# Kernel tuning notes

Hardware: AMD Instinct MI355X
Metric: run time of the kernel (lower is better)

## Reference

```python
import jax, jax.numpy as jnp
import numpy as np
import math

B, N, Q, K = 1, 64, 512, 512
C_Q = C_K = C_V = 256
C_HIDDEN = 32
NO_HEADS = 8
HID = C_HIDDEN * NO_HEADS  # 256


def setup_inputs() -> dict:
    key = jax.random.key(0)
    ks = jax.random.split(key, 12)
    inp = {
        "q_x": jax.random.normal(ks[0], (B, N, Q, C_Q), jnp.float32),
        "k_x": jax.random.normal(ks[1], (B, N, K, C_K), jnp.float32),
        "v_x": jax.random.normal(ks[2], (B, N, K, C_V), jnp.float32),
        "bias_mask": jax.random.normal(ks[3], (B, N, 1, 1, K), jnp.float32),
        "bias_pair": jax.random.normal(ks[4], (B, 1, NO_HEADS, Q, K), jnp.float32),
        # projection weights stored [in, out] (torch Linear is [out, in])
        "wq": jax.random.normal(ks[5], (C_Q, HID), jnp.float32) / math.sqrt(C_Q),
        "wk": jax.random.normal(ks[6], (C_K, HID), jnp.float32) / math.sqrt(C_K),
        "wv": jax.random.normal(ks[7], (C_V, HID), jnp.float32) / math.sqrt(C_V),
        # gating: init weights=0, bias=1 in the module; use small random for a non-trivial test
        "wg": jax.random.normal(ks[8], (C_Q, HID), jnp.float32) * 0.02,
        "bg": jnp.ones((HID,), jnp.float32),
        # output: init 'final' (zeros); use small random for a non-trivial test
        "wo": jax.random.normal(ks[9], (HID, C_Q), jnp.float32) * 0.02,
        "bo": jnp.zeros((C_Q,), jnp.float32),
    }
    return inp


def reference(q_x, k_x, v_x, bias_mask, bias_pair, wq, wk, wv, wg, bg, wo, bo):
    h, c = NO_HEADS, C_HIDDEN
    # projections -> [B, N, Q/K, H, C_h]
    q = (q_x @ wq).reshape(*q_x.shape[:-1], h, c) / math.sqrt(c)
    k = (k_x @ wk).reshape(*k_x.shape[:-1], h, c)
    v = (v_x @ wv).reshape(*v_x.shape[:-1], h, c)
    # logits [B, N, H, Q, K] with additive biases
    a = jnp.einsum("bnqhc,bnkhc->bnhqk", q, k) + bias_mask + bias_pair
    a = jax.nn.softmax(a, axis=-1)
    # output [B, N, Q, H, C_h]
    o = jnp.einsum("bnhqk,bnkhc->bnqhc", a, v)
    # gating
    g = jax.nn.sigmoid((q_x @ wg + bg).reshape(*q_x.shape[:-1], h, c))
    o = o * g
    o = o.reshape(*o.shape[:-2], h * c)
    return o @ wo + bo
```

## Files before the change

kernel.cpp:

```cpp
#include <hip/hip_runtime.h>
#include <math.h>

#define NSEQ   64
#define QLEN   512
#define KLEN   512
#define CIN    256
#define HEADS  8
#define CH     32
#define HIDDIM 256
#define M_TOTAL (NSEQ * QLEN)
#define L2E    1.4426950408889634f

typedef _Float16 f16x8 __attribute__((ext_vector_type(8)));
typedef _Float16 f16x4 __attribute__((ext_vector_type(4)));
typedef __fp16   fp16x2 __attribute__((ext_vector_type(2)));
typedef float    f32x4 __attribute__((ext_vector_type(4)));

__device__ __forceinline__ void gload16(const void* g, void* l) {
    __builtin_amdgcn_global_load_lds(
        (const __attribute__((address_space(1))) void*)g,
        (__attribute__((address_space(3))) void*)l, 16, 0, 0);
}

__device__ __forceinline__ float exp2_fast(float x) {
#if __has_builtin(__builtin_amdgcn_exp2f)
    return __builtin_amdgcn_exp2f(x);
#else
    float r; asm("v_exp_f32 %0, %1" : "=v"(r) : "v"(x)); return r;
#endif
}

__global__ __launch_bounds__(256) void wcast_kernel(
    const float* __restrict__ w0, const float* __restrict__ w1,
    const float* __restrict__ w2, const float* __restrict__ w3,
    const float* __restrict__ w4, const float* __restrict__ bm,
    float* __restrict__ bm2, _Float16* __restrict__ wt)
{
    if (blockIdx.z == 5) {
        const int id = ((blockIdx.y * 4 + blockIdx.x) * 256 + threadIdx.x) * 8;
        float4 a = *(const float4*)(bm + id);
        float4 b = *(const float4*)(bm + id + 4);
        a.x *= L2E; a.y *= L2E; a.z *= L2E; a.w *= L2E;
        b.x *= L2E; b.y *= L2E; b.z *= L2E; b.w *= L2E;
        *(float4*)(bm2 + id) = a;
        *(float4*)(bm2 + id + 4) = b;
        return;
    }
    __shared__ float t[64][65];
    const float* W;
    switch (blockIdx.z) {
        case 0: W = w0; break; case 1: W = w1; break;
        case 2: W = w2; break; case 3: W = w3; break;
        default: W = w4;
    }
    _Float16* WT = wt + (size_t)blockIdx.z * 65536;
    const int i0 = blockIdx.x * 64, o0 = blockIdx.y * 64;
    const int tid = threadIdx.x;
    const int rr = tid >> 4, c4 = tid & 15;
    #pragma unroll
    for (int i = 0; i < 4; ++i) {
        const int row = rr + i * 16;
        *(float4*)&t[row][c4 * 4] = *(const float4*)&W[(size_t)(i0 + row) * 256 + o0 + c4 * 4];
    }
    __syncthreads();
    #pragma unroll
    for (int i = 0; i < 4; ++i) {
        const int row = rr + i * 16;
        f16x4 v;
        #pragma unroll
        for (int j = 0; j < 4; ++j) v[j] = (_Float16)t[c4 * 4 + j][row];
        *(f16x4*)&WT[(size_t)(o0 + row) * 256 + i0 + c4 * 4] = v;
    }
}

__global__ __launch_bounds__(256) void bpfrag_kernel(
    const float* __restrict__ bias_pair, float* __restrict__ frag)
{
    __shared__ float t[64][68];
    const int qb = blockIdx.x, kb = blockIdx.y, h = blockIdx.z;
    const int tid = threadIdx.x;
    #pragma unroll
    for (int i = 0; i < 4; ++i) {
        const int idx = tid + i * 256;
        const int r = idx >> 4, c4 = idx & 15;
        *(float4*)&t[r][c4 * 4] = *(const float4*)
            &bias_pair[((size_t)h * QLEN + qb * 64 + r) * KLEN + kb * 64 + c4 * 4];
    }
    __syncthreads();
    const int lane = tid & 63, w = tid >> 6;
    const int l15 = lane & 15, quad = lane >> 4;
    const int qt = qb * 4 + w;
    #pragma unroll
    for (int kt2 = 0; kt2 < 4; ++kt2) {
        const int kt = kb * 4 + kt2;
        float4 v;
        v.x = (t[w * 16 + l15][kt2 * 16 + quad * 4 + 0] - 4.0f) * L2E;
        v.y = (t[w * 16 + l15][kt2 * 16 + quad * 4 + 1] - 4.0f) * L2E;
        v.z = (t[w * 16 + l15][kt2 * 16 + quad * 4 + 2] - 4.0f) * L2E;
        v.w = (t[w * 16 + l15][kt2 * 16 + quad * 4 + 3] - 4.0f) * L2E;
        *(float4*)&frag[(((size_t)(h * 32 + qt) * 32) + kt) * 256 + lane * 4] = v;
    }
}

__global__ __launch_bounds__(256, 3) void proj_gemm_kernel(
    const float* __restrict__ q_x, const float* __restrict__ k_x,
    const float* __restrict__ v_x, const _Float16* __restrict__ wT,
    const float* __restrict__ bg,
    _Float16* __restrict__ oq, _Float16* __restrict__ ok,
    _Float16* __restrict__ ovT, _Float16* __restrict__ og)
{
    __shared__ __attribute__((aligned(16))) _Float16 A_s[2][32 * 256];

    const int combo = blockIdx.x >> 7;
    const int blk   = blockIdx.x & 127;
    const int mode  = combo >> 1;
    const int nhalf = combo & 1;
    const float* A = (mode <= 1) ? q_x : (mode == 2) ? k_x : v_x;
    const _Float16* BT = wT + (size_t)mode * 65536;

    const int tid  = threadIdx.x;
    const int lane = tid & 63, w = tid >> 6;
    const int l15  = lane & 15, quad = lane >> 4;
    const int nw   = nhalf * 128 + w * 32;

    f16x8 bfr[2][8];
    #pragma unroll
    for (int nt = 0; nt < 2; ++nt)
        #pragma unroll
        for (int ks = 0; ks < 8; ++ks)
            bfr[nt][ks] = *(const f16x8*)(BT +
                (size_t)(nw + nt * 16 + l15) * 256 + ks * 32 + quad * 8);

    float4 bg4[2] = {{0.f,0.f,0.f,0.f},{0.f,0.f,0.f,0.f}};
    if (mode == 1) {
        bg4[0] = *(const float4*)&bg[nw + quad * 4];
        bg4[1] = *(const float4*)&bg[nw + 16 + quad * 4];
    }

    const int row_base = blk * 256;

    f32x4 acc[2][2];
    #pragma unroll
    for (int mt = 0; mt < 2; ++mt)
        #pragma unroll
        for (int nt = 0; nt < 2; ++nt) acc[mt][nt] = (f32x4){0.f, 0.f, 0.f, 0.f};

    float4 sreg[8];

    auto gload_panel = [&](int panel) {
        const int row0 = row_base + panel * 32;
        #pragma unroll
        for (int j = 0; j < 4; ++j) {
            const int p = tid + j * 256;
            const int r = p >> 5, c = p & 31;
            const float* ap = A + (size_t)(row0 + r) * 256 + c * 8;
            sreg[j * 2]     = *(const float4*)ap;
            sreg[j * 2 + 1] = *(const float4*)(ap + 4);
        }
    };

    auto swrite_panel = [&](int buf) {
        #pragma unroll
        for (int j = 0; j < 4; ++j) {
            const int p = tid + j * 256;
            const int r = p >> 5, c = p & 31;
            const int cp = c ^ (r & 15);
            f16x8 v;
            v[0] = (_Float16)sreg[j * 2].x;     v[1] = (_Float16)sreg[j * 2].y;
            v[2] = (_Float16)sreg[j * 2].z;     v[3] = (_Float16)sreg[j * 2].w;
            v[4] = (_Float16)sreg[j * 2 + 1].x; v[5] = (_Float16)sreg[j * 2 + 1].y;
            v[6] = (_Float16)sreg[j * 2 + 1].z; v[7] = (_Float16)sreg[j * 2 + 1].w;
            *(f16x8*)&A_s[buf][(r * 32 + cp) * 8] = v;
        }
    };

    gload_panel(0);
    swrite_panel(0);
    asm volatile("s_waitcnt lgkmcnt(0)" ::: "memory");
    __builtin_amdgcn_s_barrier();

    for (int i = 0; i < 8; ++i) {
        const int buf = i & 1;
        if (i < 7) gload_panel(i + 1);

        #pragma unroll
        for (int ks = 0; ks < 8; ++ks) {
            f16x8 af[2];
            #pragma unroll
            for (int mt = 0; mt < 2; ++mt) {
                const int r  = mt * 16 + l15;
                const int cp = (ks * 4 + quad) ^ (r & 15);
                af[mt] = *(const f16x8*)&A_s[buf][(r * 32 + cp) * 8];
            }
            if (mode != 3) {
                #pragma unroll
                for (int mt = 0; mt < 2; ++mt)
                    #pragma unroll
                    for (int nt = 0; nt < 2; ++nt)
                        acc[mt][nt] = __builtin_amdgcn_mfma_f32_16x16x32_f16(
                            bfr[nt][ks], af[mt], acc[mt][nt], 0, 0, 0);
            } else {
                #pragma unroll
                for (int mt = 0; mt < 2; ++mt)
                    #pragma unroll
                    for (int nt = 0; nt < 2; ++nt)
                        acc[mt][nt] = __builtin_amdgcn_mfma_f32_16x16x32_f16(
                            af[mt], bfr[nt][ks], acc[mt][nt], 0, 0, 0);
            }
        }

        const int row0 = row_base + i * 32;
        if (mode == 3) {
            #pragma unroll
            for (int mt = 0; mt < 2; ++mt) {
                #pragma unroll
                for (int nt = 0; nt < 2; ++nt) {
                    const int col  = nw + nt * 16 + l15;
                    const int rowg = row0 + mt * 16 + quad * 4;
                    const int nn = rowg >> 9, kpos = rowg & 511;
                    f16x4 st;
                    #pragma unroll
                    for (int reg = 0; reg < 4; ++reg) st[reg] = (_Float16)acc[mt][nt][reg];
                    *(f16x4*)&ovT[((size_t)(nn * 256 + col)) * 512 + kpos] = st;
                }
            }
        } else {
            _Float16* C = (mode == 0) ? oq : (mode == 1) ? og : ok;
            #pragma unroll
            for (int mt = 0; mt < 2; ++mt) {
                const int mrow = row0 + mt * 16 + l15;
                #pragma unroll
                for (int nt = 0; nt < 2; ++nt) {
                    const int colb = nw + nt * 16 + quad * 4;
                    f16x4 st;
                    #pragma unroll
                    for (int reg = 0; reg < 4; ++reg) {
                        float x = acc[mt][nt][reg];
                        if (mode == 0) x *= 0.2550348614f;
                        if (mode == 1) {
                            x += ((const float*)&bg4[nt])[reg];
                            x = 1.0f / (1.0f + __expf(-x));
                        }
                        st[reg] = (_Float16)x;
                    }
                    *(f16x4*)&C[(size_t)mrow * HIDDIM + colb] = st;
                }
            }
        }
        #pragma unroll
        for (int mt = 0; mt < 2; ++mt)
            #pragma unroll
            for (int nt = 0; nt < 2; ++nt) acc[mt][nt] = (f32x4){0.f, 0.f, 0.f, 0.f};

        if (i < 7) {
            swrite_panel(buf ^ 1);
            asm volatile("s_waitcnt lgkmcnt(0)" ::: "memory");
            __builtin_amdgcn_s_barrier();
        }
    }
}

__global__ __launch_bounds__(256, 4) void outproj_kernel(
    const _Float16* __restrict__ Ain, const _Float16* __restrict__ BT,
    const float* __restrict__ bias, float* __restrict__ Cout)
{
    __shared__ __attribute__((aligned(16))) _Float16 A_s[2][32 * 256];

    const int blk   = blockIdx.x & 511;
    const int nhalf = blockIdx.x >> 9;
    const int tid  = threadIdx.x;
    const int lane = tid & 63, w = tid >> 6;
    const int l15  = lane & 15, quad = lane >> 4;
    const int nw   = nhalf * 128 + w * 32;
    const int row_base = blk * 64;

    #pragma unroll
    for (int pan = 0; pan < 2; ++pan) {
        const int row0 = row_base + pan * 32;
        #pragma unroll
        for (int j = 0; j < 4; ++j) {
            const int p = tid + j * 256;
            const int r = p >> 5, c = p & 31;
            const int cl = (c & ~7) | ((c & 7) ^ (r & 7));
            gload16(Ain + (size_t)(row0 + r) * 256 + cl * 8, &A_s[pan][p * 8]);
        }
    }

    f16x8 bfr[2][8];
    #pragma unroll
    for (int nt = 0; nt < 2; ++nt)
        #pragma unroll
        for (int ks = 0; ks < 8; ++ks)
            bfr[nt][ks] = *(const f16x8*)(BT +
                (size_t)(nw + nt * 16 + l15) * 256 + ks * 32 + quad * 8);

    const float4 bias4[2] = {
        *(const float4*)&bias[nw + quad * 4],
        *(const float4*)&bias[nw + 16 + quad * 4],
    };

    __syncthreads();

    #pragma unroll
    for (int i = 0; i < 2; ++i) {
        f32x4 acc[2][2];
        #pragma unroll
        for (int mt = 0; mt < 2; ++mt)
            #pragma unroll
            for (int nt = 0; nt < 2; ++nt) acc[mt][nt] = (f32x4){0.f, 0.f, 0.f, 0.f};

        #pragma unroll
        for (int ks = 0; ks < 8; ++ks) {
            f16x8 af[2];
            #pragma unroll
            for (int mt = 0; mt < 2; ++mt) {
                const int r = mt * 16 + l15;
                const int c = (ks * 4 + quad) ^ (r & 7);
                af[mt] = *(const f16x8*)&A_s[i][r * 256 + c * 8];
            }
            #pragma unroll
            for (int mt = 0; mt < 2; ++mt)
                #pragma unroll
                for (int nt = 0; nt < 2; ++nt)
                    acc[mt][nt] = __builtin_amdgcn_mfma_f32_16x16x32_f16(
                        bfr[nt][ks], af[mt], acc[mt][nt], 0, 0, 0);
        }

        const int row0 = row_base + i * 32;
        #pragma unroll
        for (int mt = 0; mt < 2; ++mt) {
            const int mrow = row0 + mt * 16 + l15;
            #pragma unroll
            for (int nt = 0; nt < 2; ++nt) {
                const int colb = nw + nt * 16 + quad * 4;
                float4 st;
                st.x = acc[mt][nt][0] + bias4[nt].x;
                st.y = acc[mt][nt][1] + bias4[nt].y;
                st.z = acc[mt][nt][2] + bias4[nt].z;
                st.w = acc[mt][nt][3] + bias4[nt].w;
                *(float4*)&Cout[(size_t)mrow * HIDDIM + colb] = st;
            }
        }
    }
}

__global__ __launch_bounds__(256, 4) void attn_kernel(
    const _Float16* __restrict__ qb, const _Float16* __restrict__ kb,
    const _Float16* __restrict__ vT, const _Float16* __restrict__ gb,
    _Float16* __restrict__ ob,
    const float* __restrict__ bm2, const float* __restrict__ bp_frag)
{
    __shared__ _Float16 k_s[128][40];
    __shared__ _Float16 v_s[32][136];

    const int n    = blockIdx.x;
    const int h    = blockIdx.y;
    const int q0   = blockIdx.z * 128;
    const int tid  = threadIdx.x;
    const int lane = tid & 63;
    const int wq   = tid >> 6;
    const int l15  = lane & 15;
    const int quad = lane >> 4;

    f16x8 qf[2];
    #pragma unroll
    for (int qt = 0; qt < 2; ++qt)
        qf[qt] = *(const f16x8*)(qb +
            (size_t)(n * QLEN + q0 + wq * 32 + qt * 16 + l15) * HIDDIM + h * CH + quad * 8);

    const float* bpf = bp_frag +
        ((size_t)(h * 32 + blockIdx.z * 8 + wq * 2) * 32) * 256 + lane * 4;
    const float* bmb = bm2 + n * KLEN + quad * 4;

    f32x4 o_acc[2][2];
    float l_lane[2] = {0.f, 0.f};
    #pragma unroll
    for (int qt = 0; qt < 2; ++qt)
        #pragma unroll
        for (int ct = 0; ct < 2; ++ct) o_acc[qt][ct] = (f32x4){0.f, 0.f, 0.f, 0.f};

    for (int ch = 0; ch < 4; ++ch) {
        __syncthreads();
        #pragma unroll
        for (int i = 0; i < 2; ++i) {
            const int idx = tid + i * 256;
            const int r = idx >> 2, c8 = idx & 3;
            *(uint4*)&k_s[r][c8 * 8] = *(const uint4*)
                (kb + (size_t)(n * KLEN + ch * 128 + r) * HIDDIM + h * CH + c8 * 8);
            const int vr = idx >> 4, vs = idx & 15;
            *(uint4*)&v_s[vr][vs * 8] = *(const uint4*)
                (vT + ((size_t)(n * HEADS + h) * CH + vr) * KLEN + ch * 128 + vs * 8);
        }
        __syncthreads();

        #pragma unroll
        for (int kt = 0; kt < 8; ++kt) {
            const int kti = ch * 8 + kt;
            const f16x8 kf = *(const f16x8*)&k_s[kt * 16 + l15][quad * 8];
            const float4 bm  = *(const float4*)(bmb + ch * 128 + kt * 16);
            const float4 bp0 = *(const float4*)(bpf + (size_t)kti * 256);
            const float4 bp1 = *(const float4*)(bpf + (size_t)(32 + kti) * 256);
            f32x4 c0, c1;
            c0[0] = bm.x + bp0.x; c0[1] = bm.y + bp0.y;
            c0[2] = bm.z + bp0.z; c0[3] = bm.w + bp0.w;
            c1[0] = bm.x + bp1.x; c1[1] = bm.y + bp1.y;
            c1[2] = bm.z + bp1.z; c1[3] = bm.w + bp1.w;
            __builtin_amdgcn_s_setprio(1);
            const f32x4 s0 = __builtin_amdgcn_mfma_f32_16x16x32_f16(kf, qf[0], c0, 0, 0, 0);
            const f32x4 s1 = __builtin_amdgcn_mfma_f32_16x16x32_f16(kf, qf[1], c1, 0, 0, 0);
            __builtin_amdgcn_s_setprio(0);
            const f16x4 bv0 = *(const f16x4*)&v_s[l15][kt * 16 + quad * 4];
            const f16x4 bv1 = *(const f16x4*)&v_s[16 + l15][kt * 16 + quad * 4];
            #pragma unroll
            for (int qt = 0; qt < 2; ++qt) {
                const f32x4 s = qt ? s1 : s0;
                const float p0 = exp2_fast(s[0]);
                const float p1 = exp2_fast(s[1]);
                const float p2 = exp2_fast(s[2]);
                const float p3 = exp2_fast(s[3]);
                l_lane[qt] += (p0 + p1) + (p2 + p3);
                union { f16x4 v; fp16x2 h[2]; } u;
                u.h[0] = __builtin_amdgcn_cvt_pkrtz(p0, p1);
                u.h[1] = __builtin_amdgcn_cvt_pkrtz(p2, p3);
                __builtin_amdgcn_s_setprio(1);
                o_acc[qt][0] = __builtin_amdgcn_mfma_f32_16x16x16f16(u.v, bv0, o_acc[qt][0], 0, 0, 0);
                o_acc[qt][1] = __builtin_amdgcn_mfma_f32_16x16x16f16(u.v, bv1, o_acc[qt][1], 0, 0, 0);
                __builtin_amdgcn_s_setprio(0);
            }
        }
    }

    float invl[2][4];
    #pragma unroll
    for (int qt = 0; qt < 2; ++qt) {
        float lf = l_lane[qt];
        lf += __shfl_xor(lf, 16);
        lf += __shfl_xor(lf, 32);
        #pragma unroll
        for (int reg = 0; reg < 4; ++reg)
            invl[qt][reg] = 1.0f / __shfl(lf, quad * 4 + reg);
    }

    #pragma unroll
    for (int qt = 0; qt < 2; ++qt) {
        #pragma unroll
        for (int ct = 0; ct < 2; ++ct) {
            #pragma unroll
            for (int reg = 0; reg < 4; ++reg) {
                const int row = q0 + wq * 32 + qt * 16 + quad * 4 + reg;
                const size_t idx = (size_t)(n * QLEN + row) * HIDDIM + h * CH + ct * 16 + l15;
                const float g = (float)gb[idx];
                ob[idx] = (_Float16)(o_acc[qt][ct][reg] * invl[qt][reg] * g);
            }
        }
    }
}

extern "C" void kernel_launch(void* const* d_in, const int* in_sizes, int n_in,
                              void* d_out, int out_size, void* d_ws, size_t ws_size,
                              hipStream_t stream)
{
    const float* q_x       = (const float*)d_in[0];
    const float* k_x       = (const float*)d_in[1];
    const float* v_x       = (const float*)d_in[2];
    const float* bias_mask = (const float*)d_in[3];
    const float* bias_pair = (const float*)d_in[4];
    const float* wq        = (const float*)d_in[5];
    const float* wk        = (const float*)d_in[6];
    const float* wv        = (const float*)d_in[7];
    const float* wg        = (const float*)d_in[8];
    const float* bg        = (const float*)d_in[9];
    const float* wo        = (const float*)d_in[10];
    const float* bo        = (const float*)d_in[11];
    float* out = (float*)d_out;

    const size_t BUF = (size_t)M_TOTAL * HIDDIM;
    _Float16* ws_q  = (_Float16*)d_ws;
    _Float16* ws_k  = ws_q + BUF;
    _Float16* ws_vT = ws_k + BUF;
    _Float16* ws_g  = ws_vT + BUF;
    _Float16* ws_o  = ws_g + BUF;
    _Float16* wT    = ws_o + BUF;
    float*    bpf   = (float*)(wT + 5 * 65536);
    float*    bm2   = bpf + (size_t)8 * 512 * 512;

    wcast_kernel<<<dim3(4, 4, 6), 256, 0, stream>>>(
        wq, wg, wk, wv, wo, bias_mask, bm2, wT);
    bpfrag_kernel<<<dim3(8, 8, 8), 256, 0, stream>>>(bias_pair, bpf);

    proj_gemm_kernel<<<dim3(1024), 256, 0, stream>>>(
        q_x, k_x, v_x, wT, bg, ws_q, ws_k, ws_vT, ws_g);

    attn_kernel<<<dim3(NSEQ, HEADS, QLEN / 128), 256, 0, stream>>>(
        ws_q, ws_k, ws_vT, ws_g, ws_o, bm2, bpf);

    outproj_kernel<<<dim3(1024), 256, 0, stream>>>(
        ws_o, wT + 4 * 65536, bo, out);
}
```

Measured before the change: 257.5 us.

## Stream fp32 A panels into LDS via direct global loads with 4-stage pipeline

The projection GEMM now copies fp32 input rows straight into shared memory with global_load_lds, using a 4-buffer ring of 16-row panels issued three panels ahead and tracked with explicit vmcnt waits. The fp32-to-fp16 conversion moves from the staging write to the point where each fragment is read for the MFMA. This removes the register staging and the separate LDS write step and keeps more loads in flight. In exchange it uses twice the LDS per block (launch bounds drop to 2 blocks), does more conversion work per MFMA, and the hand-counted waitcnt values must match the number of loads outstanding.

```diff
diff --git a/kernel.cpp b/kernel.cpp
--- a/kernel.cpp
+++ b/kernel.cpp
@@ -102,14 +102,14 @@
     }
 }
 
-__global__ __launch_bounds__(256, 3) void proj_gemm_kernel(
+__global__ __launch_bounds__(256, 2) void proj_gemm_kernel(
     const float* __restrict__ q_x, const float* __restrict__ k_x,
     const float* __restrict__ v_x, const _Float16* __restrict__ wT,
     const float* __restrict__ bg,
     _Float16* __restrict__ oq, _Float16* __restrict__ ok,
     _Float16* __restrict__ ovT, _Float16* __restrict__ og)
 {
-    __shared__ __attribute__((aligned(16))) _Float16 A_s[2][32 * 256];
+    __shared__ __attribute__((aligned(16))) float A_s[4][16 * 256];
 
     const int combo = blockIdx.x >> 7;
     const int blk   = blockIdx.x & 127;
@@ -136,126 +136,94 @@
         bg4[0] = *(const float4*)&bg[nw + quad * 4];
         bg4[1] = *(const float4*)&bg[nw + 16 + quad * 4];
     }
+    _Float16* Cm = (mode == 0) ? oq : (mode == 1) ? og : ok;
 
     const int row_base = blk * 256;
 
-    f32x4 acc[2][2];
-    #pragma unroll
-    for (int mt = 0; mt < 2; ++mt)
-        #pragma unroll
-        for (int nt = 0; nt < 2; ++nt) acc[mt][nt] = (f32x4){0.f, 0.f, 0.f, 0.f};
-
-    float4 sreg[8];
-
-    auto gload_panel = [&](int panel) {
-        const int row0 = row_base + panel * 32;
+    auto issueL = [&](int p) {
+        const int buf = p & 3;
+        const int row0 = row_base + p * 16;
         #pragma unroll
         for (int j = 0; j < 4; ++j) {
-            const int p = tid + j * 256;
-            const int r = p >> 5, c = p & 31;
-            const float* ap = A + (size_t)(row0 + r) * 256 + c * 8;
-            sreg[j * 2]     = *(const float4*)ap;
-            sreg[j * 2 + 1] = *(const float4*)(ap + 4);
+            const int pc = tid + j * 256;
+            const int r = pc >> 6, c = pc & 63;
+            const int cl = c ^ (r & 7);
+            gload16(A + (size_t)(row0 + r) * 256 + cl * 4, &A_s[buf][pc * 4]);
         }
     };
 
-    auto swrite_panel = [&](int buf) {
-        #pragma unroll
-        for (int j = 0; j < 4; ++j) {
-            const int p = tid + j * 256;
-            const int r = p >> 5, c = p & 31;
-            const int cp = c ^ (r & 15);
-            f16x8 v;
-            v[0] = (_Float16)sreg[j * 2].x;     v[1] = (_Float16)sreg[j * 2].y;
-            v[2] = (_Float16)sreg[j * 2].z;     v[3] = (_Float16)sreg[j * 2].w;
-            v[4] = (_Float16)sreg[j * 2 + 1].x; v[5] = (_Float16)sreg[j * 2 + 1].y;
-            v[6] = (_Float16)sreg[j * 2 + 1].z; v[7] = (_Float16)sreg[j * 2 + 1].w;
-            *(f16x8*)&A_s[buf][(r * 32 + cp) * 8] = v;
-        }
-    };
-
-    gload_panel(0);
-    swrite_panel(0);
-    asm volatile("s_waitcnt lgkmcnt(0)" ::: "memory");
-    __builtin_amdgcn_s_barrier();
-
-    for (int i = 0; i < 8; ++i) {
-        const int buf = i & 1;
-        if (i < 7) gload_panel(i + 1);
+    issueL(0); issueL(1); issueL(2);
+    __builtin_amdgcn_sched_barrier(0);
+
+    #pragma unroll
+    for (int i = 0; i < 16; ++i) {
+        if (i == 0)       asm volatile("s_waitcnt vmcnt(8)"  ::: "memory");
+        else if (i == 1)  asm volatile("s_waitcnt vmcnt(10)" ::: "memory");
+        else if (i == 2)  asm volatile("s_waitcnt vmcnt(12)" ::: "memory");
+        else if (i == 14) asm volatile("s_waitcnt vmcnt(10)" ::: "memory");
+        else if (i == 15) asm volatile("s_waitcnt vmcnt(6)"  ::: "memory");
+        else              asm volatile("s_waitcnt vmcnt(14)" ::: "memory");
+        __builtin_amdgcn_sched_barrier(0);
+        __builtin_amdgcn_s_barrier();
+        __builtin_amdgcn_sched_barrier(0);
+        if (i + 3 < 16) issueL(i + 3);
+        __builtin_amdgcn_sched_barrier(0);
+
+        const int buf = i & 3;
+        f32x4 acc[2];
+        acc[0] = (f32x4){0.f, 0.f, 0.f, 0.f};
+        acc[1] = (f32x4){0.f, 0.f, 0.f, 0.f};
 
         #pragma unroll
         for (int ks = 0; ks < 8; ++ks) {
-            f16x8 af[2];
-            #pragma unroll
-            for (int mt = 0; mt < 2; ++mt) {
-                const int r  = mt * 16 + l15;
-                const int cp = (ks * 4 + quad) ^ (r & 15);
-                af[mt] = *(const f16x8*)&A_s[buf][(r * 32 + cp) * 8];
-            }
+            const int x0 = ks * 8 + ((quad * 2 + 0) ^ (l15 & 7));
+            const int x1 = ks * 8 + ((quad * 2 + 1) ^ (l15 & 7));
+            const f32x4 a0 = *(const f32x4*)&A_s[buf][l15 * 256 + x0 * 4];
+            const f32x4 a1 = *(const f32x4*)&A_s[buf][l15 * 256 + x1 * 4];
+            f16x8 af;
+            af[0] = (_Float16)a0[0]; af[1] = (_Float16)a0[1];
+            af[2] = (_Float16)a0[2]; af[3] = (_Float16)a0[3];
+            af[4] = (_Float16)a1[0]; af[5] = (_Float16)a1[1];
+            af[6] = (_Float16)a1[2]; af[7] = (_Float16)a1[3];
             if (mode != 3) {
+                acc[0] = __builtin_amdgcn_mfma_f32_16x16x32_f16(bfr[0][ks], af, acc[0], 0, 0, 0);
+                acc[1] = __builtin_amdgcn_mfma_f32_16x16x32_f16(bfr[1][ks], af, acc[1], 0, 0, 0);
+            } else {
+                acc[0] = __builtin_amdgcn_mfma_f32_16x16x32_f16(af, bfr[0][ks], acc[0], 0, 0, 0);
+                acc[1] = __builtin_amdgcn_mfma_f32_16x16x32_f16(af, bfr[1][ks], acc[1], 0, 0, 0);
+            }
+        }
+
+        const int row0 = row_base + i * 16;
+        if (mode == 3) {
+            #pragma unroll
+            for (int nt = 0; nt < 2; ++nt) {
+                const int col  = nw + nt * 16 + l15;
+                const int rowg = row0 + quad * 4;
+                const int nn = rowg >> 9, kpos = rowg & 511;
+                f16x4 st;
                 #pragma unroll
-                for (int mt = 0; mt < 2; ++mt)
-                    #pragma unroll
-                    for (int nt = 0; nt < 2; ++nt)
-                        acc[mt][nt] = __builtin_amdgcn_mfma_f32_16x16x32_f16(
-                            bfr[nt][ks], af[mt], acc[mt][nt], 0, 0, 0);
-            } else {
+                for (int reg = 0; reg < 4; ++reg) st[reg] = (_Float16)acc[nt][reg];
+                *(f16x4*)&ovT[((size_t)(nn * 256 + col)) * 512 + kpos] = st;
+            }
+        } else {
+            const int mrow = row0 + l15;
+            #pragma unroll
+            for (int nt = 0; nt < 2; ++nt) {
+                const int colb = nw + nt * 16 + quad * 4;
+                f16x4 st;
                 #pragma unroll
-                for (int mt = 0; mt < 2; ++mt)
-                    #pragma unroll
-                    for (int nt = 0; nt < 2; ++nt)
-                        acc[mt][nt] = __builtin_amdgcn_mfma_f32_16x16x32_f16(
-                            af[mt], bfr[nt][ks], acc[mt][nt], 0, 0, 0);
-            }
-        }
-
-        const int row0 = row_base + i * 32;
-        if (mode == 3) {
-            #pragma unroll
-            for (int mt = 0; mt < 2; ++mt) {
-                #pragma unroll
-                for (int nt = 0; nt < 2; ++nt) {
-                    const int col  = nw + nt * 16 + l15;
-                    const int rowg = row0 + mt * 16 + quad * 4;
-                    const int nn = rowg >> 9, kpos = rowg & 511;
-                    f16x4 st;
-                    #pragma unroll
-                    for (int reg = 0; reg < 4; ++reg) st[reg] = (_Float16)acc[mt][nt][reg];
-                    *(f16x4*)&ovT[((size_t)(nn * 256 + col)) * 512 + kpos] = st;
+                for (int reg = 0; reg < 4; ++reg) {
+                    float x = acc[nt][reg];
+                    if (mode == 0) x *= 0.2550348614f;
+                    if (mode == 1) {
+                        x += ((const float*)&bg4[nt])[reg];
+                        x = 1.0f / (1.0f + __expf(-x));
+                    }
+                    st[reg] = (_Float16)x;
                 }
-            }
-        } else {
-            _Float16* C = (mode == 0) ? oq : (mode == 1) ? og : ok;
-            #pragma unroll
-            for (int mt = 0; mt < 2; ++mt) {
-                const int mrow = row0 + mt * 16 + l15;
-                #pragma unroll
-                for (int nt = 0; nt < 2; ++nt) {
-                    const int colb = nw + nt * 16 + quad * 4;
-                    f16x4 st;
-                    #pragma unroll
-                    for (int reg = 0; reg < 4; ++reg) {
-                        float x = acc[mt][nt][reg];
-                        if (mode == 0) x *= 0.2550348614f;
-                        if (mode == 1) {
-                            x += ((const float*)&bg4[nt])[reg];
-                            x = 1.0f / (1.0f + __expf(-x));
-                        }
-                        st[reg] = (_Float16)x;
-                    }
-                    *(f16x4*)&C[(size_t)mrow * HIDDIM + colb] = st;
-                }
-            }
-        }
-        #pragma unroll
-        for (int mt = 0; mt < 2; ++mt)
-            #pragma unroll
-            for (int nt = 0; nt < 2; ++nt) acc[mt][nt] = (f32x4){0.f, 0.f, 0.f, 0.f};
-
-        if (i < 7) {
-            swrite_panel(buf ^ 1);
-            asm volatile("s_waitcnt lgkmcnt(0)" ::: "memory");
-            __builtin_amdgcn_s_barrier();
+                *(f16x4*)&Cm[(size_t)mrow * HIDDIM + colb] = st;
+            }
         }
     }
 }
```

Measured after the change: 262.1 us. About the same (+1.8%).
